# Performance work log

Hardware: AMD Instinct MI355X
Metric: run time of the kernel (lower is better)

The kernel has to match this reference:

```python
import jax, jax.numpy as jnp
import numpy as np

N_NODES = 100000
N_EDGES = 1200000
N_GRAPHS = 1024
IN_DIM, HIDDEN, OUT_DIM = 4, 64, 2
BN_EPS = 1e-5


def setup_inputs() -> dict:
    key = jax.random.key(0)
    ks = jax.random.split(key, 12)
    x = jax.random.normal(ks[0], (N_NODES, IN_DIM), dtype=jnp.float32)
    edge_index = jax.random.randint(ks[1], (2, N_EDGES), 0, N_NODES, dtype=jnp.int64)
    batch = jnp.sort(jax.random.randint(ks[2], (N_NODES,), 0, N_GRAPHS, dtype=jnp.int64))
    s = 1.0 / np.sqrt(HIDDEN)
    return {
        "x": x,
        "edge_index": edge_index,
        "batch": batch,
        "W_enc": jax.random.normal(ks[3], (IN_DIM, HIDDEN), dtype=jnp.float32) * 0.5,
        "b_enc": jnp.zeros((HIDDEN,), dtype=jnp.float32),
        "bn_gamma": jnp.ones((HIDDEN,), dtype=jnp.float32),
        "bn_beta": jnp.zeros((HIDDEN,), dtype=jnp.float32),
        "bn_mean": jax.random.normal(ks[4], (HIDDEN,), dtype=jnp.float32) * 0.1,
        "bn_var": jax.random.uniform(ks[5], (HIDDEN,), dtype=jnp.float32, minval=0.5, maxval=1.5),
        "W_gcn": jax.random.normal(ks[6], (HIDDEN, HIDDEN), dtype=jnp.float32) * s,
        "b_gcn": jnp.zeros((HIDDEN,), dtype=jnp.float32),
        "W_cls1": jax.random.normal(ks[7], (HIDDEN, HIDDEN), dtype=jnp.float32) * s,
        "b_cls1": jnp.zeros((HIDDEN,), dtype=jnp.float32),
        "W_cls2": jax.random.normal(ks[8], (HIDDEN, OUT_DIM), dtype=jnp.float32) * s,
        "b_cls2": jnp.zeros((OUT_DIM,), dtype=jnp.float32),
    }


def reference(x, edge_index, batch, W_enc, b_enc, bn_gamma, bn_beta, bn_mean, bn_var,
              W_gcn, b_gcn, W_cls1, b_cls1, W_cls2, b_cls2):
    n = x.shape[0]
    # Encoder: Linear -> ReLU -> Dropout(eval=identity) -> BatchNorm1d (running stats)
    h = jnp.maximum(x @ W_enc + b_enc, 0.0)
    h = (h - bn_mean) * jax.lax.rsqrt(bn_var + BN_EPS) * bn_gamma + bn_beta
    # GCNConv (PyG): add self-loops, symmetric deg^{-1/2} normalization
    loop = jnp.arange(n, dtype=edge_index.dtype)
    src = jnp.concatenate([edge_index[0], loop])  # [E+N]
    dst = jnp.concatenate([edge_index[1], loop])
    deg = jnp.zeros((n,), dtype=h.dtype).at[dst].add(1.0)
    dis = jnp.where(deg > 0, jax.lax.rsqrt(jnp.maximum(deg, 1.0)), 0.0)
    norm = dis[src] * dis[dst]  # [E+N]
    hw = h @ W_gcn  # [N, H]
    msg = hw[src] * norm[:, None]  # gather + scale, [E+N, H]
    agg = jax.ops.segment_sum(msg, dst, num_segments=n) + b_gcn
    agg = jnp.maximum(agg, 0.0)  # .relu()
    # global_mean_pool over graphs
    sums = jax.ops.segment_sum(agg, batch, num_segments=N_GRAPHS)  # [G, H]
    cnts = jax.ops.segment_sum(jnp.ones((n,), dtype=agg.dtype), batch, num_segments=N_GRAPHS)
    gm = sums / jnp.maximum(cnts, 1.0)[:, None]
    # Classifier: Linear -> ReLU -> Dropout(eval) -> Linear
    out = jnp.maximum(gm @ W_cls1 + b_cls1, 0.0) @ W_cls2 + b_cls2
    return out
```

## Files before the change

kernel.cpp:

```cpp
#include <hip/hip_runtime.h>

#define N_NODES  100000
#define N_EDGES  1200000
#define N_GRAPHS 1024

#define BUCK_SHIFT 10
#define BUCK_NODES 1024
#define NBUCK 98
#define FBLK  256
#define CHUNK ((N_EDGES + FBLK - 1) / FBLK)

__device__ __forceinline__ unsigned short f2bf(float f) {
  unsigned u = __float_as_uint(f);
  return (unsigned short)((u + 0x7fffu + ((u >> 16) & 1u)) >> 16);
}
__device__ __forceinline__ float bf2f(unsigned short b) {
  return __uint_as_float(((unsigned)b) << 16);
}

__global__ __launch_bounds__(256) void k_cnt(const int* __restrict__ ei,
                                             int* __restrict__ cnt,
                                             float* __restrict__ gsum) {
  __shared__ int h[NBUCK];
  int t = threadIdx.x;
  for (int i = t; i < NBUCK; i += 256) h[i] = 0;
  for (int i = blockIdx.x * 256 + t; i < N_GRAPHS * 64; i += FBLK * 256) gsum[i] = 0.f;
  __syncthreads();
  int start = blockIdx.x * CHUNK, end = min(start + CHUNK, N_EDGES);
  for (int e = start + t; e < end; e += 256)
    atomicAdd(&h[ei[N_EDGES + e] >> BUCK_SHIFT], 1);
  __syncthreads();
  for (int b = t; b < NBUCK; b += 256)
    cnt[b * FBLK + blockIdx.x] = h[b];
}

__global__ __launch_bounds__(256) void k_colscan(int* __restrict__ cnt,
                                                 int* __restrict__ tot) {
  __shared__ int wsum[4];
  int b = blockIdx.x, t = threadIdx.x;
  int v = cnt[b * FBLK + t];
  int lane = t & 63, w = t >> 6;
  int incl = v;
  #pragma unroll
  for (int off = 1; off < 64; off <<= 1) {
    int y = __shfl_up(incl, off);
    if (lane >= off) incl += y;
  }
  if (lane == 63) wsum[w] = incl;
  __syncthreads();
  if (t == 0) {
    int s = 0;
    #pragma unroll
    for (int i = 0; i < 4; ++i) { int x = wsum[i]; wsum[i] = s; s += x; }
    tot[b] = s;
  }
  __syncthreads();
  cnt[b * FBLK + t] = wsum[w] + incl - v;
}

__global__ void k_base(const int* __restrict__ tot, int* __restrict__ base) {
  __shared__ int s[128];
  int t = threadIdx.x;
  int v = (t < NBUCK) ? tot[t] : 0;
  s[t] = v;
  __syncthreads();
  for (int off = 1; off < 128; off <<= 1) {
    int x = (t >= off) ? s[t - off] : 0;
    __syncthreads();
    s[t] += x;
    __syncthreads();
  }
  if (t < NBUCK) base[t] = s[t] - v;
  if (t == 0) base[NBUCK] = N_EDGES;
}

__global__ __launch_bounds__(256) void k_fill(const int* __restrict__ ei,
                                              const int* __restrict__ cnt,
                                              const int* __restrict__ base,
                                              int* __restrict__ binned) {
  __shared__ int cur[NBUCK];
  int t = threadIdx.x, blk = blockIdx.x;
  for (int b = t; b < NBUCK; b += 256) cur[b] = base[b] + cnt[b * FBLK + blk];
  __syncthreads();
  int start = blk * CHUNK, end = min(start + CHUNK, N_EDGES);
  for (int e = start + t; e < end; e += 256) {
    int src = ei[e];
    int dst = ei[N_EDGES + e];
    int b = dst >> BUCK_SHIFT;
    int p = atomicAdd(&cur[b], 1);
    binned[p] = src | ((dst & (BUCK_NODES - 1)) << 17);
  }
}

__global__ __launch_bounds__(512) void k_csr(const int* __restrict__ base,
                                             const int* __restrict__ binned,
                                             int* __restrict__ csr,
                                             int* __restrict__ row_start,
                                             float* __restrict__ dis) {
  __shared__ int hist[BUCK_NODES];
  __shared__ int rs[BUCK_NODES];
  __shared__ int wsum[8];
  int t = threadIdx.x;
  int blk = blockIdx.x;
  int b0 = base[blk];
  int nE = base[blk + 1] - b0;
  int node0 = blk << BUCK_SHIFT;
  int nNodes = min(BUCK_NODES, N_NODES - node0);
  hist[t] = 0; hist[t + 512] = 0;
  __syncthreads();
  for (int i = t; i < nE; i += 512)
    atomicAdd(&hist[(unsigned)binned[b0 + i] >> 17], 1);
  __syncthreads();
  int x0 = hist[2 * t], x1 = hist[2 * t + 1];
  int a = x0 + x1;
  int lane = t & 63, w = t >> 6;
  int incl = a;
  #pragma unroll
  for (int off = 1; off < 64; off <<= 1) {
    int y = __shfl_up(incl, off);
    if (lane >= off) incl += y;
  }
  if (lane == 63) wsum[w] = incl;
  __syncthreads();
  if (w == 0) {
    int v = (lane < 8) ? wsum[lane] : 0;
    for (int off = 1; off < 8; off <<= 1) {
      int y = __shfl_up(v, off);
      if (lane >= off) v += y;
    }
    if (lane < 8) wsum[lane] = v;
  }
  __syncthreads();
  int woff = (w > 0) ? wsum[w - 1] : 0;
  int exclPair = woff + incl - a;
  rs[2 * t] = exclPair;
  rs[2 * t + 1] = exclPair + x0;
  __syncthreads();
  for (int n = t; n < BUCK_NODES; n += 512) {
    int cnt_n = ((n < BUCK_NODES - 1) ? rs[n + 1] : nE) - rs[n];
    hist[n] = rs[n];
    if (n < nNodes) {
      row_start[node0 + n] = b0 + rs[n];
      dis[node0 + n] = rsqrtf((float)(cnt_n + 1));
    }
  }
  if (t == 0 && blk == NBUCK - 1) row_start[N_NODES] = N_EDGES;
  __syncthreads();
  for (int i = t; i < nE; i += 512) {
    int v = binned[b0 + i];
    int d = (unsigned)v >> 17;
    int p = atomicAdd(&hist[d], 1);
    csr[b0 + p] = v & 0x1FFFF;
  }
}

__global__ __launch_bounds__(256) void k_enc(
    const float* __restrict__ x,
    const float* __restrict__ Wenc, const float* __restrict__ benc,
    const float* __restrict__ gamma, const float* __restrict__ beta,
    const float* __restrict__ mean,  const float* __restrict__ var,
    const float* __restrict__ Wgcn,  const float* __restrict__ dis,
    unsigned short* __restrict__ hws) {
  int lane = threadIdx.x & 63;
  int wv = (blockIdx.x * 256 + threadIdx.x) >> 6;
  float be = benc[lane];
  float sc = gamma[lane] * rsqrtf(var[lane] + 1e-5f);
  float mu = mean[lane], bt = beta[lane];
  float w0 = Wenc[lane], w1 = Wenc[64 + lane], w2 = Wenc[128 + lane], w3 = Wenc[192 + lane];
  float wreg[64];
  #pragma unroll
  for (int k = 0; k < 64; ++k) wreg[k] = Wgcn[k * 64 + lane];
  int n0 = wv * 16;
  for (int i = 0; i < 16; ++i) {
    int n = n0 + i;
    float4 xv = ((const float4*)x)[n];
    float h = fmaf(xv.w, w3, fmaf(xv.z, w2, fmaf(xv.y, w1, fmaf(xv.x, w0, be))));
    h = fmaxf(h, 0.f);
    float hbn = (h - mu) * sc + bt;
    int hb = __float_as_int(hbn);
    float a0 = 0.f, a1 = 0.f, a2 = 0.f, a3 = 0.f;
    #pragma unroll
    for (int k = 0; k < 64; k += 4) {
      a0 = fmaf(__int_as_float(__builtin_amdgcn_readlane(hb, k)),     wreg[k],     a0);
      a1 = fmaf(__int_as_float(__builtin_amdgcn_readlane(hb, k + 1)), wreg[k + 1], a1);
      a2 = fmaf(__int_as_float(__builtin_amdgcn_readlane(hb, k + 2)), wreg[k + 2], a2);
      a3 = fmaf(__int_as_float(__builtin_amdgcn_readlane(hb, k + 3)), wreg[k + 3], a3);
    }
    float acc = ((a0 + a1) + (a2 + a3)) * dis[n];
    hws[(size_t)n * 64 + lane] = f2bf(acc);
  }
}

__global__ __launch_bounds__(256) void k_gather(
    const int* __restrict__ row_start, const int* __restrict__ csr,
    const float* __restrict__ dis, const unsigned short* __restrict__ hws,
    const int* __restrict__ batch, const float* __restrict__ bgcn,
    float* __restrict__ gsum) {
  int lane = threadIdx.x & 63;
  int wv = blockIdx.x * 4 + (threadIdx.x >> 6);
  int nb = wv * 4;
  if (nb >= N_NODES) return;
  float bias = bgcn[lane];
  float vout[4];
  int gid[4];
  #pragma unroll
  for (int k = 0; k < 4; ++k) {
    int n = nb + k;
    int st = row_start[n], en = row_start[n + 1];
    float dn = dis[n];
    float a0 = 0.f, a1 = 0.f, a2 = 0.f, a3 = 0.f;
    for (int c = st; c < en; c += 64) {
      int idx = c + lane;
      int sj = (idx < en) ? csr[idx] : 0;
      int m = min(64, en - c);
      int j = 0;
      for (; j + 4 <= m; j += 4) {
        int s0 = __shfl(sj, j), s1 = __shfl(sj, j + 1);
        int s2 = __shfl(sj, j + 2), s3 = __shfl(sj, j + 3);
        a0 += bf2f(hws[(size_t)s0 * 64 + lane]);
        a1 += bf2f(hws[(size_t)s1 * 64 + lane]);
        a2 += bf2f(hws[(size_t)s2 * 64 + lane]);
        a3 += bf2f(hws[(size_t)s3 * 64 + lane]);
      }
      for (; j < m; ++j) {
        int s = __shfl(sj, j);
        a0 += bf2f(hws[(size_t)s * 64 + lane]);
      }
    }
    float self = bf2f(hws[(size_t)n * 64 + lane]);
    vout[k] = fmaxf(dn * (((a0 + a1) + (a2 + a3)) + self) + bias, 0.f);
    gid[k] = batch[n];
  }
  float vs = vout[0];
  int cg = gid[0];
  #pragma unroll
  for (int k = 1; k < 4; ++k) {
    if (gid[k] == cg) vs += vout[k];
    else {
      atomicAdd(&gsum[cg * 64 + lane], vs);
      vs = vout[k]; cg = gid[k];
    }
  }
  atomicAdd(&gsum[cg * 64 + lane], vs);
}

__global__ void k_cls(const float* __restrict__ gsum, const int* __restrict__ batch,
                      const float* __restrict__ W1, const float* __restrict__ b1,
                      const float* __restrict__ W2, const float* __restrict__ b2,
                      float* __restrict__ out) {
  __shared__ float gm[64];
  __shared__ int cntS;
  int j = threadIdx.x;
  int g = blockIdx.x;
  if (j == 0) {
    int lo = 0, hi = N_NODES;
    while (lo < hi) { int mid = (lo + hi) >> 1; if (batch[mid] < g) lo = mid + 1; else hi = mid; }
    int lo2 = lo, hi2 = N_NODES;
    while (lo2 < hi2) { int mid = (lo2 + hi2) >> 1; if (batch[mid] < g + 1) lo2 = mid + 1; else hi2 = mid; }
    cntS = lo2 - lo;
  }
  __syncthreads();
  float denom = fmaxf((float)cntS, 1.0f);
  gm[j] = gsum[g * 64 + j] / denom;
  __syncthreads();
  float hid = b1[j];
  #pragma unroll
  for (int k = 0; k < 64; ++k) hid += gm[k] * W1[k * 64 + j];
  hid = fmaxf(hid, 0.f);
  float o0 = hid * W2[j * 2 + 0];
  float o1 = hid * W2[j * 2 + 1];
  #pragma unroll
  for (int off = 32; off > 0; off >>= 1) {
    o0 += __shfl_down(o0, off);
    o1 += __shfl_down(o1, off);
  }
  if (j == 0) {
    out[g * 2 + 0] = o0 + b2[0];
    out[g * 2 + 1] = o1 + b2[1];
  }
}

extern "C" void kernel_launch(void* const* d_in, const int* in_sizes, int n_in,
                              void* d_out, int out_size, void* d_ws, size_t ws_size,
                              hipStream_t stream) {
  const float* x     = (const float*)d_in[0];
  const int*   ei    = (const int*)d_in[1];
  const int*   batch = (const int*)d_in[2];
  const float* Wenc  = (const float*)d_in[3];
  const float* benc  = (const float*)d_in[4];
  const float* gamma = (const float*)d_in[5];
  const float* beta  = (const float*)d_in[6];
  const float* mean  = (const float*)d_in[7];
  const float* var   = (const float*)d_in[8];
  const float* Wgcn  = (const float*)d_in[9];
  const float* bgcn  = (const float*)d_in[10];
  const float* W1    = (const float*)d_in[11];
  const float* b1    = (const float*)d_in[12];
  const float* W2    = (const float*)d_in[13];
  const float* b2    = (const float*)d_in[14];
  float* out = (float*)d_out;

  char* ws = (char*)d_ws;
  float*          gsum      = (float*)ws;          ws += (size_t)N_GRAPHS * 64 * 4;
  int*            cnt       = (int*)ws;            ws += (size_t)NBUCK * FBLK * 4;
  int*            tot       = (int*)ws;            ws += 128 * 4;
  int*            basep     = (int*)ws;            ws += 128 * 4;
  int*            binned    = (int*)ws;            ws += (size_t)N_EDGES * 4;
  int*            csr       = (int*)ws;            ws += (size_t)N_EDGES * 4;
  int*            row_start = (int*)ws;            ws += (size_t)(N_NODES + 32) * 4;
  float*          dis       = (float*)ws;          ws += (size_t)N_NODES * 4;
  unsigned short* hws       = (unsigned short*)ws; ws += (size_t)N_NODES * 64 * 2;

  k_cnt<<<FBLK, 256, 0, stream>>>(ei, cnt, gsum);
  k_colscan<<<NBUCK, 256, 0, stream>>>(cnt, tot);
  k_base<<<1, 128, 0, stream>>>(tot, basep);
  k_fill<<<FBLK, 256, 0, stream>>>(ei, cnt, basep, binned);
  k_csr<<<NBUCK, 512, 0, stream>>>(basep, binned, csr, row_start, dis);
  k_enc<<<(N_NODES / 16 + 3) / 4, 256, 0, stream>>>(x, Wenc, benc, gamma, beta, mean, var,
                                                    Wgcn, dis, hws);
  k_gather<<<(N_NODES / 16), 256, 0, stream>>>(row_start, csr, dis, hws, batch, bgcn, gsum);
  k_cls<<<N_GRAPHS, 64, 0, stream>>>(gsum, batch, W1, b1, W2, b2, out);
}
```

Measured before the change: 206.2 us.

## Merge CSR build launches via cooperative kernel and decouple encoder from degree scaling

The edge bucket count is fused with the node encoder into one launch. The encoder no longer depends on the degree normalisation, so it can run before the CSR is built. The column scan, base scan and bucket fill are merged into a single cooperative kernel that uses grid-wide syncs, which removes several small launches. The source-side degree scaling moves into the gather loop as an extra per-edge dis lookup and fma, so the gather does more work in exchange for fewer launches and serial dependencies.

```diff
diff --git a/kernel.cpp b/kernel.cpp
--- a/kernel.cpp
+++ b/kernel.cpp
@@ -1,4 +1,7 @@
 #include <hip/hip_runtime.h>
+#include <hip/hip_cooperative_groups.h>
+
+namespace cg = cooperative_groups;
 
 #define N_NODES  100000
 #define N_EDGES  1200000
@@ -9,6 +12,7 @@
 #define NBUCK 98
 #define FBLK  256
 #define CHUNK ((N_EDGES + FBLK - 1) / FBLK)
+#define ENC_BLOCKS 1563
 
 __device__ __forceinline__ unsigned short f2bf(float f) {
   unsigned u = __float_as_uint(f);
@@ -18,151 +22,31 @@
   return __uint_as_float(((unsigned)b) << 16);
 }
 
-__global__ __launch_bounds__(256) void k_cnt(const int* __restrict__ ei,
-                                             int* __restrict__ cnt,
-                                             float* __restrict__ gsum) {
-  __shared__ int h[NBUCK];
-  int t = threadIdx.x;
-  for (int i = t; i < NBUCK; i += 256) h[i] = 0;
-  for (int i = blockIdx.x * 256 + t; i < N_GRAPHS * 64; i += FBLK * 256) gsum[i] = 0.f;
-  __syncthreads();
-  int start = blockIdx.x * CHUNK, end = min(start + CHUNK, N_EDGES);
-  for (int e = start + t; e < end; e += 256)
-    atomicAdd(&h[ei[N_EDGES + e] >> BUCK_SHIFT], 1);
-  __syncthreads();
-  for (int b = t; b < NBUCK; b += 256)
-    cnt[b * FBLK + blockIdx.x] = h[b];
-}
-
-__global__ __launch_bounds__(256) void k_colscan(int* __restrict__ cnt,
-                                                 int* __restrict__ tot) {
-  __shared__ int wsum[4];
-  int b = blockIdx.x, t = threadIdx.x;
-  int v = cnt[b * FBLK + t];
-  int lane = t & 63, w = t >> 6;
-  int incl = v;
-  #pragma unroll
-  for (int off = 1; off < 64; off <<= 1) {
-    int y = __shfl_up(incl, off);
-    if (lane >= off) incl += y;
-  }
-  if (lane == 63) wsum[w] = incl;
-  __syncthreads();
-  if (t == 0) {
-    int s = 0;
-    #pragma unroll
-    for (int i = 0; i < 4; ++i) { int x = wsum[i]; wsum[i] = s; s += x; }
-    tot[b] = s;
-  }
-  __syncthreads();
-  cnt[b * FBLK + t] = wsum[w] + incl - v;
-}
-
-__global__ void k_base(const int* __restrict__ tot, int* __restrict__ base) {
-  __shared__ int s[128];
-  int t = threadIdx.x;
-  int v = (t < NBUCK) ? tot[t] : 0;
-  s[t] = v;
-  __syncthreads();
-  for (int off = 1; off < 128; off <<= 1) {
-    int x = (t >= off) ? s[t - off] : 0;
-    __syncthreads();
-    s[t] += x;
-    __syncthreads();
-  }
-  if (t < NBUCK) base[t] = s[t] - v;
-  if (t == 0) base[NBUCK] = N_EDGES;
-}
-
-__global__ __launch_bounds__(256) void k_fill(const int* __restrict__ ei,
-                                              const int* __restrict__ cnt,
-                                              const int* __restrict__ base,
-                                              int* __restrict__ binned) {
-  __shared__ int cur[NBUCK];
-  int t = threadIdx.x, blk = blockIdx.x;
-  for (int b = t; b < NBUCK; b += 256) cur[b] = base[b] + cnt[b * FBLK + blk];
-  __syncthreads();
-  int start = blk * CHUNK, end = min(start + CHUNK, N_EDGES);
-  for (int e = start + t; e < end; e += 256) {
-    int src = ei[e];
-    int dst = ei[N_EDGES + e];
-    int b = dst >> BUCK_SHIFT;
-    int p = atomicAdd(&cur[b], 1);
-    binned[p] = src | ((dst & (BUCK_NODES - 1)) << 17);
-  }
-}
-
-__global__ __launch_bounds__(512) void k_csr(const int* __restrict__ base,
-                                             const int* __restrict__ binned,
-                                             int* __restrict__ csr,
-                                             int* __restrict__ row_start,
-                                             float* __restrict__ dis) {
-  __shared__ int hist[BUCK_NODES];
-  __shared__ int rs[BUCK_NODES];
-  __shared__ int wsum[8];
-  int t = threadIdx.x;
-  int blk = blockIdx.x;
-  int b0 = base[blk];
-  int nE = base[blk + 1] - b0;
-  int node0 = blk << BUCK_SHIFT;
-  int nNodes = min(BUCK_NODES, N_NODES - node0);
-  hist[t] = 0; hist[t + 512] = 0;
-  __syncthreads();
-  for (int i = t; i < nE; i += 512)
-    atomicAdd(&hist[(unsigned)binned[b0 + i] >> 17], 1);
-  __syncthreads();
-  int x0 = hist[2 * t], x1 = hist[2 * t + 1];
-  int a = x0 + x1;
-  int lane = t & 63, w = t >> 6;
-  int incl = a;
-  #pragma unroll
-  for (int off = 1; off < 64; off <<= 1) {
-    int y = __shfl_up(incl, off);
-    if (lane >= off) incl += y;
-  }
-  if (lane == 63) wsum[w] = incl;
-  __syncthreads();
-  if (w == 0) {
-    int v = (lane < 8) ? wsum[lane] : 0;
-    for (int off = 1; off < 8; off <<= 1) {
-      int y = __shfl_up(v, off);
-      if (lane >= off) v += y;
-    }
-    if (lane < 8) wsum[lane] = v;
-  }
-  __syncthreads();
-  int woff = (w > 0) ? wsum[w - 1] : 0;
-  int exclPair = woff + incl - a;
-  rs[2 * t] = exclPair;
-  rs[2 * t + 1] = exclPair + x0;
-  __syncthreads();
-  for (int n = t; n < BUCK_NODES; n += 512) {
-    int cnt_n = ((n < BUCK_NODES - 1) ? rs[n + 1] : nE) - rs[n];
-    hist[n] = rs[n];
-    if (n < nNodes) {
-      row_start[node0 + n] = b0 + rs[n];
-      dis[node0 + n] = rsqrtf((float)(cnt_n + 1));
-    }
-  }
-  if (t == 0 && blk == NBUCK - 1) row_start[N_NODES] = N_EDGES;
-  __syncthreads();
-  for (int i = t; i < nE; i += 512) {
-    int v = binned[b0 + i];
-    int d = (unsigned)v >> 17;
-    int p = atomicAdd(&hist[d], 1);
-    csr[b0 + p] = v & 0x1FFFF;
-  }
-}
-
-__global__ __launch_bounds__(256) void k_enc(
+__global__ __launch_bounds__(256) void k_front(
+    const int* __restrict__ ei, int* __restrict__ cnt, float* __restrict__ gsum,
     const float* __restrict__ x,
     const float* __restrict__ Wenc, const float* __restrict__ benc,
     const float* __restrict__ gamma, const float* __restrict__ beta,
     const float* __restrict__ mean,  const float* __restrict__ var,
-    const float* __restrict__ Wgcn,  const float* __restrict__ dis,
-    unsigned short* __restrict__ hws) {
-  int lane = threadIdx.x & 63;
-  int wv = (blockIdx.x * 256 + threadIdx.x) >> 6;
+    const float* __restrict__ Wgcn,
+    unsigned short* __restrict__ hw) {
+  int t = threadIdx.x;
+  if (blockIdx.x < FBLK) {
+    __shared__ int h[NBUCK];
+    for (int i = t; i < NBUCK; i += 256) h[i] = 0;
+    gsum[blockIdx.x * 256 + t] = 0.f;
+    __syncthreads();
+    int start = blockIdx.x * CHUNK, end = min(start + CHUNK, N_EDGES);
+    for (int e = start + t; e < end; e += 256)
+      atomicAdd(&h[ei[N_EDGES + e] >> BUCK_SHIFT], 1);
+    __syncthreads();
+    for (int b = t; b < NBUCK; b += 256)
+      cnt[b * FBLK + blockIdx.x] = h[b];
+    return;
+  }
+  int lane = t & 63;
+  int wv = ((blockIdx.x - FBLK) * 256 + t) >> 6;
+  if (wv >= 6250) return;
   float be = benc[lane];
   float sc = gamma[lane] * rsqrtf(var[lane] + 1e-5f);
   float mu = mean[lane], bt = beta[lane];
@@ -186,14 +70,132 @@
       a2 = fmaf(__int_as_float(__builtin_amdgcn_readlane(hb, k + 2)), wreg[k + 2], a2);
       a3 = fmaf(__int_as_float(__builtin_amdgcn_readlane(hb, k + 3)), wreg[k + 3], a3);
     }
-    float acc = ((a0 + a1) + (a2 + a3)) * dis[n];
-    hws[(size_t)n * 64 + lane] = f2bf(acc);
+    hw[(size_t)n * 64 + lane] = f2bf((a0 + a1) + (a2 + a3));
+  }
+}
+
+__global__ __launch_bounds__(256) void k_build(int* __restrict__ cnt,
+                                               int* __restrict__ tot,
+                                               int* __restrict__ base,
+                                               const int* __restrict__ ei,
+                                               int* __restrict__ binned) {
+  cg::grid_group grid = cg::this_grid();
+  int t = threadIdx.x, blk = blockIdx.x;
+  int lane = t & 63, w = t >> 6;
+  if (blk < NBUCK) {
+    __shared__ int wsum[4];
+    int v = cnt[blk * FBLK + t];
+    int incl = v;
+    #pragma unroll
+    for (int off = 1; off < 64; off <<= 1) {
+      int y = __shfl_up(incl, off);
+      if (lane >= off) incl += y;
+    }
+    if (lane == 63) wsum[w] = incl;
+    __syncthreads();
+    if (t == 0) {
+      int s = 0;
+      #pragma unroll
+      for (int i = 0; i < 4; ++i) { int x2 = wsum[i]; wsum[i] = s; s += x2; }
+      tot[blk] = s;
+    }
+    __syncthreads();
+    cnt[blk * FBLK + t] = wsum[w] + incl - v;
+  }
+  grid.sync();
+  if (blk == 0) {
+    __shared__ int s[256];
+    int v = (t < NBUCK) ? tot[t] : 0;
+    s[t] = v;
+    __syncthreads();
+    for (int off = 1; off < 256; off <<= 1) {
+      int x2 = (t >= off) ? s[t - off] : 0;
+      __syncthreads();
+      s[t] += x2;
+      __syncthreads();
+    }
+    if (t < NBUCK) base[t] = s[t] - v;
+    if (t == 0) base[NBUCK] = N_EDGES;
+  }
+  grid.sync();
+  __shared__ int cur[NBUCK];
+  for (int b = t; b < NBUCK; b += 256) cur[b] = base[b] + cnt[b * FBLK + blk];
+  __syncthreads();
+  int start = blk * CHUNK, end = min(start + CHUNK, N_EDGES);
+  for (int e = start + t; e < end; e += 256) {
+    int src = ei[e];
+    int dst = ei[N_EDGES + e];
+    int b = dst >> BUCK_SHIFT;
+    int p = atomicAdd(&cur[b], 1);
+    binned[p] = src | ((dst & (BUCK_NODES - 1)) << 17);
+  }
+}
+
+__global__ __launch_bounds__(512) void k_csr(const int* __restrict__ base,
+                                             const int* __restrict__ binned,
+                                             int* __restrict__ csr,
+                                             int* __restrict__ row_start,
+                                             float* __restrict__ dis) {
+  __shared__ int hist[BUCK_NODES];
+  __shared__ int rs[BUCK_NODES];
+  __shared__ int wsum[8];
+  int t = threadIdx.x;
+  int blk = blockIdx.x;
+  int b0 = base[blk];
+  int nE = base[blk + 1] - b0;
+  int node0 = blk << BUCK_SHIFT;
+  int nNodes = min(BUCK_NODES, N_NODES - node0);
+  hist[t] = 0; hist[t + 512] = 0;
+  __syncthreads();
+  for (int i = t; i < nE; i += 512)
+    atomicAdd(&hist[(unsigned)binned[b0 + i] >> 17], 1);
+  __syncthreads();
+  int x0 = hist[2 * t], x1 = hist[2 * t + 1];
+  int a = x0 + x1;
+  int lane = t & 63, w = t >> 6;
+  int incl = a;
+  #pragma unroll
+  for (int off = 1; off < 64; off <<= 1) {
+    int y = __shfl_up(incl, off);
+    if (lane >= off) incl += y;
+  }
+  if (lane == 63) wsum[w] = incl;
+  __syncthreads();
+  if (w == 0) {
+    int v = (lane < 8) ? wsum[lane] : 0;
+    for (int off = 1; off < 8; off <<= 1) {
+      int y = __shfl_up(v, off);
+      if (lane >= off) v += y;
+    }
+    if (lane < 8) wsum[lane] = v;
+  }
+  __syncthreads();
+  int woff = (w > 0) ? wsum[w - 1] : 0;
+  int exclPair = woff + incl - a;
+  rs[2 * t] = exclPair;
+  rs[2 * t + 1] = exclPair + x0;
+  __syncthreads();
+  for (int n = t; n < BUCK_NODES; n += 512) {
+    int cnt_n = ((n < BUCK_NODES - 1) ? rs[n + 1] : nE) - rs[n];
+    hist[n] = rs[n];
+    if (n < nNodes) {
+      row_start[node0 + n] = b0 + rs[n];
+      dis[node0 + n] = rsqrtf((float)(cnt_n + 1));
+    }
+  }
+  if (t == 0 && blk == NBUCK - 1) row_start[N_NODES] = N_EDGES;
+  __syncthreads();
+  for (int i = t; i < nE; i += 512) {
+    int v = binned[b0 + i];
+    int d = (unsigned)v >> 17;
+    int p = atomicAdd(&hist[d], 1);
+    csr[b0 + p] = v & 0x1FFFF;
   }
 }
 
 __global__ __launch_bounds__(256) void k_gather(
     const int* __restrict__ row_start, const int* __restrict__ csr,
-    const float* __restrict__ dis, const unsigned short* __restrict__ hws,
+    const float* __restrict__ dis, const unsigned short* __restrict__ hw,
     const int* __restrict__ batch, const float* __restrict__ bgcn,
     float* __restrict__ gsum) {
   int lane = threadIdx.x & 63;
@@ -211,37 +213,41 @@
     float a0 = 0.f, a1 = 0.f, a2 = 0.f, a3 = 0.f;
     for (int c = st; c < en; c += 64) {
       int idx = c + lane;
-      int sj = (idx < en) ? csr[idx] : 0;
+      int sj = 0; float dj = 0.f;
+      if (idx < en) { sj = csr[idx]; dj = dis[sj]; }
       int m = min(64, en - c);
       int j = 0;
       for (; j + 4 <= m; j += 4) {
         int s0 = __shfl(sj, j), s1 = __shfl(sj, j + 1);
         int s2 = __shfl(sj, j + 2), s3 = __shfl(sj, j + 3);
-        a0 += bf2f(hws[(size_t)s0 * 64 + lane]);
-        a1 += bf2f(hws[(size_t)s1 * 64 + lane]);
-        a2 += bf2f(hws[(size_t)s2 * 64 + lane]);
-        a3 += bf2f(hws[(size_t)s3 * 64 + lane]);
+        float d0 = __shfl(dj, j), d1 = __shfl(dj, j + 1);
+        float d2 = __shfl(dj, j + 2), d3 = __shfl(dj, j + 3);
+        a0 = fmaf(d0, bf2f(hw[(size_t)s0 * 64 + lane]), a0);
+        a1 = fmaf(d1, bf2f(hw[(size_t)s1 * 64 + lane]), a1);
+        a2 = fmaf(d2, bf2f(hw[(size_t)s2 * 64 + lane]), a2);
+        a3 = fmaf(d3, bf2f(hw[(size_t)s3 * 64 + lane]), a3);
       }
       for (; j < m; ++j) {
         int s = __shfl(sj, j);
-        a0 += bf2f(hws[(size_t)s * 64 + lane]);
+        float d = __shfl(dj, j);
+        a0 = fmaf(d, bf2f(hw[(size_t)s * 64 + lane]), a0);
       }
     }
-    float self = bf2f(hws[(size_t)n * 64 + lane]);
-    vout[k] = fmaxf(dn * (((a0 + a1) + (a2 + a3)) + self) + bias, 0.f);
+    float self = bf2f(hw[(size_t)n * 64 + lane]);
+    vout[k] = fmaxf(dn * (((a0 + a1) + (a2 + a3)) + dn * self) + bias, 0.f);
     gid[k] = batch[n];
   }
   float vs = vout[0];
-  int cg = gid[0];
+  int cg_ = gid[0];
   #pragma unroll
   for (int k = 1; k < 4; ++k) {
-    if (gid[k] == cg) vs += vout[k];
+    if (gid[k] == cg_) vs += vout[k];
     else {
-      atomicAdd(&gsum[cg * 64 + lane], vs);
-      vs = vout[k]; cg = gid[k];
-    }
-  }
-  atomicAdd(&gsum[cg * 64 + lane], vs);
+      atomicAdd(&gsum[cg_ * 64 + lane], vs);
+      vs = vout[k]; cg_ = gid[k];
+    }
+  }
+  atomicAdd(&gsum[cg_ * 64 + lane], vs);
 }
 
 __global__ void k_cls(const float* __restrict__ gsum, const int* __restrict__ batch,
@@ -309,15 +315,15 @@
   int*            csr       = (int*)ws;            ws += (size_t)N_EDGES * 4;
   int*            row_start = (int*)ws;            ws += (size_t)(N_NODES + 32) * 4;
   float*          dis       = (float*)ws;          ws += (size_t)N_NODES * 4;
-  unsigned short* hws       = (unsigned short*)ws; ws += (size_t)N_NODES * 64 * 2;
-
-  k_cnt<<<FBLK, 256, 0, stream>>>(ei, cnt, gsum);
-  k_colscan<<<NBUCK, 256, 0, stream>>>(cnt, tot);
-  k_base<<<1, 128, 0, stream>>>(tot, basep);
-  k_fill<<<FBLK, 256, 0, stream>>>(ei, cnt, basep, binned);
+  unsigned short* hw        = (unsigned short*)ws; ws += (size_t)N_NODES * 64 * 2;
+
+  k_front<<<FBLK + ENC_BLOCKS, 256, 0, stream>>>(ei, cnt, gsum, x, Wenc, benc, gamma,
+                                                 beta, mean, var, Wgcn, hw);
+  {
+    void* args[] = {(void*)&cnt, (void*)&tot, (void*)&basep, (void*)&ei, (void*)&binned};
+    hipLaunchCooperativeKernel((void*)k_build, dim3(FBLK), dim3(256), args, 0, stream);
+  }
   k_csr<<<NBUCK, 512, 0, stream>>>(basep, binned, csr, row_start, dis);
-  k_enc<<<(N_NODES / 16 + 3) / 4, 256, 0, stream>>>(x, Wenc, benc, gamma, beta, mean, var,
-                                                    Wgcn, dis, hws);
-  k_gather<<<(N_NODES / 16), 256, 0, stream>>>(row_start, csr, dis, hws, batch, bgcn, gsum);
+  k_gather<<<(N_NODES / 16), 256, 0, stream>>>(row_start, csr, dis, hw, batch, bgcn, gsum);
   k_cls<<<N_GRAPHS, 64, 0, stream>>>(gsum, batch, W1, b1, W2, b2, out);
 }
```

Result: slower. 278.5 us (+35.1%).
